# Optimization experiments

Hardware: AMD Instinct MI355X
Metric: run time of the kernel (lower is better)

The kernel has to match this reference:

```python
import jax, jax.numpy as jnp
import numpy as np

N_SRC, N_MID, N_TGT = 200000, 100000, 50000
E1, E2 = 1600000, 800000
D_IN, D_HID, D_OUT = 128, 256, 64


def setup_inputs() -> dict:
    key = jax.random.key(0)
    ks = jax.random.split(key, 10)
    x = jax.random.normal(ks[0], (N_SRC, D_IN), dtype=jnp.float32)
    # edge_index[0] = source node ids, edge_index[1] = target node ids (PyG source_to_target)
    ei1 = jnp.stack([
        jax.random.randint(ks[1], (E1,), 0, N_SRC, dtype=jnp.int32),
        jax.random.randint(ks[2], (E1,), 0, N_MID, dtype=jnp.int32),
    ])
    ei2 = jnp.stack([
        jax.random.randint(ks[3], (E2,), 0, N_MID, dtype=jnp.int32),
        jax.random.randint(ks[4], (E2,), 0, N_TGT, dtype=jnp.int32),
    ])
    s = 1.0 / np.sqrt(D_IN)
    Wl1 = jax.random.uniform(ks[5], (D_IN, D_HID), jnp.float32, -s, s)
    Wr1 = jax.random.uniform(ks[6], (D_IN, D_HID), jnp.float32, -s, s)
    b1 = jnp.zeros((D_HID,), jnp.float32)
    s2 = 1.0 / np.sqrt(D_HID)
    Wl2 = jax.random.uniform(ks[7], (D_HID, D_OUT), jnp.float32, -s2, s2)
    Wr2 = jax.random.uniform(ks[8], (D_HID, D_OUT), jnp.float32, -s2, s2)
    b2 = jnp.zeros((D_OUT,), jnp.float32)
    return {"x": x, "edge_index1": ei1, "edge_index2": ei2,
            "Wl1": Wl1, "Wr1": Wr1, "b1": b1,
            "Wl2": Wl2, "Wr2": Wr2, "b2": b2}


def _sage_conv(x_src, x_tgt, edge_index, Wl, Wr, b, n_tgt):
    # mean aggregation of source features onto targets, then two linear branches
    msg = x_src[edge_index[0]]                                   # [E, d]
    agg = jax.ops.segment_sum(msg, edge_index[1], num_segments=n_tgt)
    cnt = jax.ops.segment_sum(jnp.ones((edge_index.shape[1],), x_src.dtype),
                              edge_index[1], num_segments=n_tgt)
    agg = agg / jnp.maximum(cnt, 1.0)[:, None]
    return agg @ Wl + x_tgt @ Wr + b


def reference(x, edge_index1, edge_index2, Wl1, Wr1, b1, Wl2, Wr2, b2):
    # layer 1: [N_SRC, D_IN] -> [N_MID, D_HID], then ReLU (dropout inactive in eval)
    h = _sage_conv(x, x[:N_MID], edge_index1, Wl1, Wr1, b1, N_MID)
    h = jax.nn.relu(h)
    # layer 2 (final): no activation
    out = _sage_conv(h, h[:N_TGT], edge_index2, Wl2, Wr2, b2, N_TGT)
    return out
```

## Files before the change

### kernel.cpp

```cpp
#include <hip/hip_runtime.h>


#define NSRC 200000
#define NMID 100000
#define NTGT 50000
#define NE1  1600000
#define NE2  800000
#define DIN  128
#define DHID 256
#define DOUT 64

#define XCH (NSRC * 16)

#define CH   4096
#define NBK1 391
#define NBK2 196
#define NCH1 ((NE1 + CH - 1) / CH)
#define NCH2 ((NE2 + CH - 1) / CH)
#define HCH  8192
#define NHC1 ((NE1 + HCH - 1) / HCH)
#define NHC2 ((NE2 + HCH - 1) / HCH)
#define MAXBUF 6144

typedef __attribute__((ext_vector_type(8))) short bf16x8;
typedef __attribute__((ext_vector_type(4))) float f32x4;
typedef __attribute__((ext_vector_type(2))) float f32x2;

__device__ __forceinline__ unsigned short f2bf(float f) {
    unsigned int u = __builtin_bit_cast(unsigned int, f);
    u += 0x7FFFu + ((u >> 16) & 1u);
    return (unsigned short)(u >> 16);
}
__device__ __forceinline__ float bf_lo(unsigned int u) {
    return __builtin_bit_cast(float, u << 16);
}
__device__ __forceinline__ float bf_hi(unsigned int u) {
    return __builtin_bit_cast(float, u & 0xFFFF0000u);
}

__global__ __launch_bounds__(256) void convert_all_kernel(
    const float* __restrict__ x,
    const float* __restrict__ Wl1, const float* __restrict__ Wr1,
    const float* __restrict__ Wl2, const float* __restrict__ Wr2,
    unsigned short* __restrict__ xb, unsigned short* __restrict__ WT1,
    unsigned short* __restrict__ WT2)
{
    int gid = blockIdx.x * 256 + threadIdx.x;
    if (gid < XCH) {
        const float4 v0 = *(const float4*)(x + (long long)gid * 8);
        const float4 v1 = *(const float4*)(x + (long long)gid * 8 + 4);
        unsigned short o[8] = {f2bf(v0.x), f2bf(v0.y), f2bf(v0.z), f2bf(v0.w),
                               f2bf(v1.x), f2bf(v1.y), f2bf(v1.z), f2bf(v1.w)};
        *(uint4*)(xb + (long long)gid * 8) = *(const uint4*)o;
        return;
    }
    int g = gid - XCH;
    if (g < 65536) {
        int n = g >> 8, k = g & 255;
        float v = (k < DIN) ? Wl1[(long long)k * DHID + n]
                            : Wr1[(long long)(k - DIN) * DHID + n];
        WT1[g] = f2bf(v);
        return;
    }
    g -= 65536;
    if (g < 32768) {
        int n2 = g >> 8, k = g & 255;
        float v = (n2 < DOUT) ? Wl2[(long long)k * DOUT + n2]
                              : Wr2[(long long)k * DOUT + (n2 - DOUT)];
        WT2[g] = f2bf(v);
    }
}


__global__ __launch_bounds__(256) void bucket_hist_kernel(
    const int* __restrict__ ei1, const int* __restrict__ ei2,
    int* __restrict__ bhist1, int* __restrict__ bhist2)
{
    __shared__ unsigned int lh[512];
    const int* ei; int* bh; int nE, nbk, chunk;
    if (blockIdx.x < NHC1) { ei = ei1; bh = bhist1; nE = NE1; nbk = NBK1; chunk = blockIdx.x; }
    else { ei = ei2; bh = bhist2; nE = NE2; nbk = NBK2; chunk = blockIdx.x - NHC1; }
    int t = threadIdx.x;
    lh[t] = 0; lh[t + 256] = 0;
    __syncthreads();
    int base = chunk * HCH;
    int end = nE < base + HCH ? nE : base + HCH;
    for (int e = base + t; e < end; e += 256)
        atomicAdd(&lh[((unsigned)ei[nE + e]) >> 8], 1u);
    __syncthreads();
    if (t < nbk && lh[t]) atomicAdd(&bh[t], (int)lh[t]);
    if (t + 256 < nbk && lh[t + 256]) atomicAdd(&bh[t + 256], (int)lh[t + 256]);
}

__global__ __launch_bounds__(256) void bucket_scan_kernel(
    const int* __restrict__ bhist1, const int* __restrict__ bhist2,
    int* __restrict__ bbase1, int* __restrict__ bbase2,
    int* __restrict__ bcur1, int* __restrict__ bcur2,
    int* __restrict__ rs1, int* __restrict__ rs2)
{
    __shared__ int s[256];
    int t = threadIdx.x;
    int a0 = (2 * t < NBK1) ? bhist1[2 * t] : 0;
    int a1 = (2 * t + 1 < NBK1) ? bhist1[2 * t + 1] : 0;
    s[t] = a0 + a1;
    __syncthreads();
    for (int off = 1; off < 256; off <<= 1) {
        int u = (t >= off) ? s[t - off] : 0;
        __syncthreads();
        s[t] += u;
        __syncthreads();
    }
    int ex = (t > 0) ? s[t - 1] : 0;
    if (2 * t < NBK1)     { bbase1[2 * t] = ex;      bcur1[2 * t] = ex; }
    if (2 * t + 1 < NBK1) { bbase1[2 * t + 1] = ex + a0; bcur1[2 * t + 1] = ex + a0; }
    if (t == 0) { bbase1[NBK1] = NE1; rs1[NMID] = NE1; bbase2[NBK2] = NE2; rs2[NTGT] = NE2; }
    __syncthreads();
    int b0 = (t < NBK2) ? bhist2[t] : 0;
    s[t] = b0;
    __syncthreads();
    for (int off = 1; off < 256; off <<= 1) {
        int u = (t >= off) ? s[t - off] : 0;
        __syncthreads();
        s[t] += u;
        __syncthreads();
    }
    int ex2 = (t > 0) ? s[t - 1] : 0;
    if (t < NBK2) { bbase2[t] = ex2; bcur2[t] = ex2; }
}

__global__ __launch_bounds__(256) void bin_kernel(
    const int* __restrict__ ei1, const int* __restrict__ ei2,
    int* __restrict__ bcur1, int* __restrict__ bcur2,
    uint2* __restrict__ gbuf1, uint2* __restrict__ gbuf2)
{
    __shared__ unsigned int lcnt[512];
    __shared__ unsigned int lofs[512];
    __shared__ unsigned int lpos[512];
    __shared__ unsigned int gbase[512];
    __shared__ unsigned int swarp[256];
    __shared__ uint2 lbuf[CH];

    const int* ei; int* bcur; uint2* gbuf; int nE, nbk, chunk;
    if (blockIdx.x < NCH1) {
        ei = ei1; bcur = bcur1; gbuf = gbuf1; nE = NE1; nbk = NBK1; chunk = blockIdx.x;
    } else {
        ei = ei2; bcur = bcur2; gbuf = gbuf2; nE = NE2; nbk = NBK2; chunk = blockIdx.x - NCH1;
    }
    int base = chunk * CH;
    int nb = nE - base; if (nb > CH) nb = CH;
    int t = threadIdx.x;

    for (int i = t; i < 512; i += 256) { lcnt[i] = 0; lpos[i] = 0; }
    __syncthreads();

    int srcv[16], tgtv[16];
    #pragma unroll
    for (int i = 0; i < 16; ++i) {
        int e = base + i * 256 + t;
        if (e < nE) {
            tgtv[i] = ei[nE + e];
            srcv[i] = ei[e];
            atomicAdd(&lcnt[tgtv[i] >> 8], 1u);
        } else tgtv[i] = -1;
    }
    __syncthreads();

    unsigned a0 = lcnt[2 * t], a1 = lcnt[2 * t + 1];
    swarp[t] = a0 + a1;
    __syncthreads();
    for (int off = 1; off < 256; off <<= 1) {
        unsigned v = (t >= off) ? swarp[t - off] : 0;
        __syncthreads();
        swarp[t] += v;
        __syncthreads();
    }
    unsigned ex = (t > 0) ? swarp[t - 1] : 0;
    lofs[2 * t] = ex;
    lofs[2 * t + 1] = ex + a0;
    if (2 * t < nbk && a0) gbase[2 * t] = atomicAdd(&bcur[2 * t], (int)a0);
    if (2 * t + 1 < nbk && a1) gbase[2 * t + 1] = atomicAdd(&bcur[2 * t + 1], (int)a1);
    __syncthreads();

    #pragma unroll
    for (int i = 0; i < 16; ++i) {
        if (tgtv[i] >= 0) {
            int b = tgtv[i] >> 8;
            unsigned idx = lofs[b] + atomicAdd(&lpos[b], 1u);
            lbuf[idx] = make_uint2((unsigned)srcv[i], (unsigned)tgtv[i]);
        }
    }
    __syncthreads();

    for (int i = t; i < nb; i += 256) {
        uint2 r = lbuf[i];
        int b = (int)(r.y >> 8);
        unsigned gi = gbase[b] + ((unsigned)i - lofs[b]);
        gbuf[gi] = r;
    }
}

__global__ __launch_bounds__(256) void bucket_csr_kernel(
    const uint2* __restrict__ gbuf1, const uint2* __restrict__ gbuf2,
    const int* __restrict__ bbase1, const int* __restrict__ bbase2,
    int* __restrict__ rs1, int* __restrict__ rs2,
    int* __restrict__ csr1, int* __restrict__ csr2)
{
    __shared__ unsigned int lhist[256];
    __shared__ unsigned int lcur[256];
    __shared__ unsigned int sscan[256];
    __shared__ unsigned int lbuf[MAXBUF];
    const uint2* gbuf; const int* bbase; int* rs; int* csr; int bucket, ntot;
    if (blockIdx.x < NBK1) {
        gbuf = gbuf1; bbase = bbase1; rs = rs1; csr = csr1; bucket = blockIdx.x; ntot = NMID;
    } else {
        gbuf = gbuf2; bbase = bbase2; rs = rs2; csr = csr2; bucket = blockIdx.x - NBK1; ntot = NTGT;
    }
    int base = bbase[bucket];
    int size = bbase[bucket + 1] - base;
    int node0 = bucket << 8;
    int nnode = ntot - node0; if (nnode > 256) nnode = 256;
    int t = threadIdx.x;
    lhist[t] = 0;
    __syncthreads();
    for (int i = t; i < size; i += 256)
        atomicAdd(&lhist[gbuf[base + i].y & 255], 1u);
    __syncthreads();
    unsigned v = lhist[t];
    sscan[t] = v;
    __syncthreads();
    for (int off = 1; off < 256; off <<= 1) {
        unsigned u = (t >= off) ? sscan[t - off] : 0;
        __syncthreads();
        sscan[t] += u;
        __syncthreads();
    }
    unsigned ex = (t > 0) ? sscan[t - 1] : 0;
    lcur[t] = ex;
    if (t < nnode) rs[node0 + t] = base + (int)ex;
    __syncthreads();
    for (int i = t; i < size; i += 256) {
        uint2 r = gbuf[base + i];
        unsigned pos = atomicAdd(&lcur[r.y & 255], 1u);
        lbuf[pos] = r.x;
    }
    __syncthreads();
    for (int i = t; i < size; i += 256)
        csr[base + i] = (int)lbuf[i];
}


__global__ __launch_bounds__(256) void gather1_kernel(
    const unsigned short* __restrict__ xb, const int* __restrict__ rs,
    const int* __restrict__ csr, unsigned short* __restrict__ aggnb)
{
    int wid = threadIdx.x >> 6;
    int lane = threadIdx.x & 63;
    int node = __builtin_amdgcn_readfirstlane(blockIdx.x * 4 + wid);
    if (node >= NMID) return;
    int s = rs[node];
    int d = rs[node + 1] - s;
    const unsigned int* xw = (const unsigned int*)xb;
    f32x2 a0 = {0.f, 0.f}, a1 = {0.f, 0.f}, a2 = {0.f, 0.f}, a3 = {0.f, 0.f};
    int j = 0;
    for (; j + 3 < d; j += 4) {
        int i0 = csr[s + j];
        int i1 = csr[s + j + 1];
        int i2 = csr[s + j + 2];
        int i3 = csr[s + j + 3];
        unsigned int u0 = xw[((size_t)(unsigned)i0 << 6) + lane];
        unsigned int u1 = xw[((size_t)(unsigned)i1 << 6) + lane];
        unsigned int u2 = xw[((size_t)(unsigned)i2 << 6) + lane];
        unsigned int u3 = xw[((size_t)(unsigned)i3 << 6) + lane];
        a0 += (f32x2){bf_lo(u0), bf_hi(u0)};
        a1 += (f32x2){bf_lo(u1), bf_hi(u1)};
        a2 += (f32x2){bf_lo(u2), bf_hi(u2)};
        a3 += (f32x2){bf_lo(u3), bf_hi(u3)};
    }
    for (; j < d; ++j) {
        int i0 = csr[s + j];
        unsigned int u0 = xw[((size_t)(unsigned)i0 << 6) + lane];
        a0 += (f32x2){bf_lo(u0), bf_hi(u0)};
    }
    float inv = (d > 0) ? 1.0f / (float)d : 0.f;
    f32x2 r = (a0 + a1) + (a2 + a3);
    float r0 = r.x * inv;
    float r1 = r.y * inv;
    unsigned int packed = (unsigned int)f2bf(r0) | ((unsigned int)f2bf(r1) << 16);
    *(unsigned int*)(aggnb + (long long)node * DIN + lane * 2) = packed;
}

__global__ __launch_bounds__(256) void gather2_final_kernel(
    const float* __restrict__ p, const float* __restrict__ qb,
    const int* __restrict__ rs, const int* __restrict__ csr,
    float* __restrict__ out)
{
    int wid = threadIdx.x >> 6;
    int lane = threadIdx.x & 63;
    int node = __builtin_amdgcn_readfirstlane(blockIdx.x * 4 + wid);
    if (node >= NTGT) return;
    int s = rs[node];
    int d = rs[node + 1] - s;
    float a0 = 0.f, a1 = 0.f, a2 = 0.f, a3 = 0.f;
    int j = 0;
    for (; j + 3 < d; j += 4) {
        int i0 = csr[s + j];
        int i1 = csr[s + j + 1];
        int i2 = csr[s + j + 2];
        int i3 = csr[s + j + 3];
        a0 += p[((size_t)(unsigned)i0 << 6) + lane];
        a1 += p[((size_t)(unsigned)i1 << 6) + lane];
        a2 += p[((size_t)(unsigned)i2 << 6) + lane];
        a3 += p[((size_t)(unsigned)i3 << 6) + lane];
    }
    for (; j < d; ++j) {
        int i0 = csr[s + j];
        a0 += p[((size_t)(unsigned)i0 << 6) + lane];
    }
    float inv = (d > 0) ? 1.0f / (float)d : 0.f;
    out[(long long)node * DOUT + lane] =
        qb[(long long)node * DOUT + lane] + ((a0 + a1) + (a2 + a3)) * inv;
}

#define LDSP 40

__global__ __launch_bounds__(256) void gemm1_mfma(
    const unsigned short* __restrict__ aggnb, const unsigned short* __restrict__ xb,
    const unsigned short* __restrict__ WT, const float* __restrict__ bias,
    unsigned short* __restrict__ h)
{
    __shared__ unsigned short Asm[128 * LDSP];
    __shared__ unsigned short Bsm[128 * LDSP];
    const int tid = threadIdx.x;
    const int bm = blockIdx.x * 128;
    const int bn = blockIdx.y * 128;
    const int wave = tid >> 6, lane = tid & 63;
    const int wr = wave >> 1, wc = wave & 1;
    const int lrow = lane & 15, quad = lane >> 4;

    const int c0r = tid >> 2, c0s = tid & 3;
    const int c1r = (tid + 256) >> 2, c1s = tid & 3;
    int growA0 = bm + c0r; if (growA0 >= NMID) growA0 = NMID - 1;
    int growA1 = bm + c1r; if (growA1 >= NMID) growA1 = NMID - 1;

    uint4 pa0, pa1, pb0, pb1;
    auto gload = [&](int k0) {
        int gk0 = k0 + c0s * 8;
        const unsigned short* sA0 = (gk0 < DIN)
            ? (aggnb + (long long)growA0 * DIN + gk0)
            : (xb + (long long)growA0 * DIN + (gk0 - DIN));
        pa0 = *(const uint4*)sA0;
        const unsigned short* sA1 = (gk0 < DIN)
            ? (aggnb + (long long)growA1 * DIN + gk0)
            : (xb + (long long)growA1 * DIN + (gk0 - DIN));
        pa1 = *(const uint4*)sA1;
        pb0 = *(const uint4*)(WT + (long long)(bn + c0r) * 256 + k0 + c0s * 8);
        pb1 = *(const uint4*)(WT + (long long)(bn + c1r) * 256 + k0 + c1s * 8);
    };

    f32x4 acc[4][4];
    #pragma unroll
    for (int i = 0; i < 4; ++i)
        #pragma unroll
        for (int j = 0; j < 4; ++j)
            acc[i][j] = (f32x4){0.f, 0.f, 0.f, 0.f};

    gload(0);
    for (int it = 0; it < 8; ++it) {
        if (it) __syncthreads();
        *(uint4*)(Asm + c0r * LDSP + c0s * 8) = pa0;
        *(uint4*)(Asm + c1r * LDSP + c1s * 8) = pa1;
        *(uint4*)(Bsm + c0r * LDSP + c0s * 8) = pb0;
        *(uint4*)(Bsm + c1r * LDSP + c1s * 8) = pb1;
        __syncthreads();
        if (it < 7) gload((it + 1) * 32);
        bf16x8 af[4], bfr[4];
        #pragma unroll
        for (int mi = 0; mi < 4; ++mi)
            af[mi] = *(const bf16x8*)(Asm + (wr * 64 + mi * 16 + lrow) * LDSP + quad * 8);
        #pragma unroll
        for (int ni = 0; ni < 4; ++ni)
            bfr[ni] = *(const bf16x8*)(Bsm + (wc * 64 + ni * 16 + lrow) * LDSP + quad * 8);
        #pragma unroll
        for (int mi = 0; mi < 4; ++mi)
            #pragma unroll
            for (int ni = 0; ni < 4; ++ni)
                acc[mi][ni] = __builtin_amdgcn_mfma_f32_16x16x32_bf16(
                    af[mi], bfr[ni], acc[mi][ni], 0, 0, 0);
    }
    #pragma unroll
    for (int mi = 0; mi < 4; ++mi) {
        #pragma unroll
        for (int ni = 0; ni < 4; ++ni) {
            int col = bn + wc * 64 + ni * 16 + lrow;
            float bv = bias[col];
            #pragma unroll
            for (int r = 0; r < 4; ++r) {
                int row = bm + wr * 64 + mi * 16 + quad * 4 + r;
                if (row < NMID) {
                    float v = acc[mi][ni][r] + bv;
                    h[(long long)row * DHID + col] = f2bf(fmaxf(v, 0.0f));
                }
            }
        }
    }
}

__global__ __launch_bounds__(256) void gemm2_dual_mfma(
    const unsigned short* __restrict__ h, const unsigned short* __restrict__ WT2,
    const float* __restrict__ b2,
    float* __restrict__ p, float* __restrict__ qb)
{
    __shared__ unsigned short Asm[128 * LDSP];
    __shared__ unsigned short Bsm[128 * LDSP];
    const int tid = threadIdx.x;
    const int bm = blockIdx.x * 128;
    const int wave = tid >> 6, lane = tid & 63;
    const int lrow = lane & 15, quad = lane >> 4;
    const bool doq = (bm < NTGT);

    const int c0r = tid >> 2, c0s = tid & 3;
    const int c1r = (tid + 256) >> 2;
    int growA0 = bm + c0r; if (growA0 >= NMID) growA0 = NMID - 1;
    int growA1 = bm + c1r; if (growA1 >= NMID) growA1 = NMID - 1;

    uint4 pa0, pa1, pb0, pb1;
    auto gload = [&](int k0) {
        pa0 = *(const uint4*)(h + (long long)growA0 * DHID + k0 + c0s * 8);
        pa1 = *(const uint4*)(h + (long long)growA1 * DHID + k0 + c0s * 8);
        pb0 = *(const uint4*)(WT2 + (long long)c0r * 256 + k0 + c0s * 8);
        pb1 = *(const uint4*)(WT2 + (long long)c1r * 256 + k0 + c0s * 8);
    };

    f32x4 accP[2][4], accQ[2][4];
    #pragma unroll
    for (int i = 0; i < 2; ++i)
        #pragma unroll
        for (int j = 0; j < 4; ++j) {
            accP[i][j] = (f32x4){0.f, 0.f, 0.f, 0.f};
            accQ[i][j] = (f32x4){0.f, 0.f, 0.f, 0.f};
        }

    gload(0);
    for (int it = 0; it < 8; ++it) {
        if (it) __syncthreads();
        *(uint4*)(Asm + c0r * LDSP + c0s * 8) = pa0;
        *(uint4*)(Asm + c1r * LDSP + c0s * 8) = pa1;
        *(uint4*)(Bsm + c0r * LDSP + c0s * 8) = pb0;
        *(uint4*)(Bsm + c1r * LDSP + c0s * 8) = pb1;
        __syncthreads();
        if (it < 7) gload((it + 1) * 32);
        bf16x8 af[2], bp[4];
        #pragma unroll
        for (int mi = 0; mi < 2; ++mi)
            af[mi] = *(const bf16x8*)(Asm + (wave * 32 + mi * 16 + lrow) * LDSP + quad * 8);
        #pragma unroll
        for (int ni = 0; ni < 4; ++ni)
            bp[ni] = *(const bf16x8*)(Bsm + (ni * 16 + lrow) * LDSP + quad * 8);
        #pragma unroll
        for (int mi = 0; mi < 2; ++mi)
            #pragma unroll
            for (int ni = 0; ni < 4; ++ni)
                accP[mi][ni] = __builtin_amdgcn_mfma_f32_16x16x32_bf16(
                    af[mi], bp[ni], accP[mi][ni], 0, 0, 0);
        if (doq) {
            bf16x8 bq[4];
            #pragma unroll
            for (int ni = 0; ni < 4; ++ni)
                bq[ni] = *(const bf16x8*)(Bsm + (64 + ni * 16 + lrow) * LDSP + quad * 8);
            #pragma unroll
            for (int mi = 0; mi < 2; ++mi)
                #pragma unroll
                for (int ni = 0; ni < 4; ++ni)
                    accQ[mi][ni] = __builtin_amdgcn_mfma_f32_16x16x32_bf16(
                        af[mi], bq[ni], accQ[mi][ni], 0, 0, 0);
        }
    }
    #pragma unroll
    for (int mi = 0; mi < 2; ++mi) {
        #pragma unroll
        for (int ni = 0; ni < 4; ++ni) {
            int col = ni * 16 + lrow;
            #pragma unroll
            for (int r = 0; r < 4; ++r) {
                int row = bm + wave * 32 + mi * 16 + quad * 4 + r;
                if (row < NMID)
                    p[(long long)row * DOUT + col] = accP[mi][ni][r];
                if (doq && row < NTGT)
                    qb[(long long)row * DOUT + col] = accQ[mi][ni][r] + b2[col];
            }
        }
    }
}

extern "C" void kernel_launch(void* const* d_in, const int* in_sizes, int n_in,
                              void* d_out, int out_size, void* d_ws, size_t ws_size,
                              hipStream_t stream) {
    const float* x   = (const float*)d_in[0];
    const int*   ei1 = (const int*)d_in[1];
    const int*   ei2 = (const int*)d_in[2];
    const float* Wl1 = (const float*)d_in[3];
    const float* Wr1 = (const float*)d_in[4];
    const float* b1  = (const float*)d_in[5];
    const float* Wl2 = (const float*)d_in[6];
    const float* Wr2 = (const float*)d_in[7];
    const float* b2  = (const float*)d_in[8];
    float* out = (float*)d_out;

    unsigned short* xb    = (unsigned short*)d_ws;
    unsigned short* aggnb = xb + (size_t)NSRC * DIN;
    unsigned short* h     = aggnb + (size_t)NMID * DIN;
    unsigned short* WT1   = h + (size_t)NMID * DHID;
    unsigned short* WT2   = WT1 + 256 * 256;
    float* p    = (float*)(WT2 + 128 * 256);
    float* qb   = p + (size_t)NMID * DOUT;
    int* rs1    = (int*)(qb + (size_t)NTGT * DOUT);
    int* rs2    = rs1 + (NMID + 1);
    int* bhist1 = rs2 + (NTGT + 1);
    int* bhist2 = bhist1 + NBK1;
    int* bbase1 = bhist2 + NBK2;
    int* bbase2 = bbase1 + (NBK1 + 1);
    int* bcur1  = bbase2 + (NBK2 + 1);
    int* bcur2  = bcur1 + NBK1;
    int* csr1   = bcur2 + NBK2 + 1;
    int* csr2   = csr1 + NE1;
    uint2* gbuf1 = (uint2*)(((size_t)(csr2 + NE2) + 15) & ~(size_t)15);
    uint2* gbuf2 = gbuf1 + NE1;

    convert_all_kernel<<<(XCH + 65536 + 32768 + 255) / 256, 256, 0, stream>>>(
        x, Wl1, Wr1, Wl2, Wr2, xb, WT1, WT2);

    hipMemsetAsync(bhist1, 0, (size_t)(NBK1 + NBK2) * 4, stream);
    bucket_hist_kernel<<<NHC1 + NHC2, 256, 0, stream>>>(ei1, ei2, bhist1, bhist2);
    bucket_scan_kernel<<<1, 256, 0, stream>>>(bhist1, bhist2, bbase1, bbase2,
                                              bcur1, bcur2, rs1, rs2);
    bin_kernel<<<NCH1 + NCH2, 256, 0, stream>>>(ei1, ei2, bcur1, bcur2, gbuf1, gbuf2);
    bucket_csr_kernel<<<NBK1 + NBK2, 256, 0, stream>>>(
        gbuf1, gbuf2, bbase1, bbase2, rs1, rs2, csr1, csr2);

    gather1_kernel<<<(NMID + 3) / 4, 256, 0, stream>>>(xb, rs1, csr1, aggnb);
    {
        dim3 grid((NMID + 127) / 128, 2);
        gemm1_mfma<<<grid, 256, 0, stream>>>(aggnb, xb, WT1, b1, h);
    }
    gemm2_dual_mfma<<<(NMID + 127) / 128, 256, 0, stream>>>(h, WT2, b2, p, qb);
    gather2_final_kernel<<<(NTGT + 3) / 4, 256, 0, stream>>>(p, qb, rs2, csr2, out);
}
```

Baseline: 404.9 us.

## Make gather kernels persistent with 8-way unrolled loads and prefetched row ranges

Both gather kernels now launch a fixed grid of 2048 blocks, and each wave grid-strides over nodes instead of handling one node per wave. The next node's row start and end are prefetched while the current node is processed. The inner loop is unrolled to 8 independent loads, and the remainder is handled by a masked 8-wide tail block. This aims to raise memory-level parallelism and cut block scheduling overhead. The costs are possible over-reads of csr past a node's range, extra redundant loads in the tail, and lower occupancy.

```diff
diff --git a/kernel.cpp b/kernel.cpp
--- a/kernel.cpp
+++ b/kernel.cpp
@@ -22,6 +22,9 @@
 #define NHC2 ((NE2 + HCH - 1) / HCH)
 #define MAXBUF 6144
 
+#define GBLK 2048
+#define WSTRIDE (GBLK * 4)
+
 typedef __attribute__((ext_vector_type(8))) short bf16x8;
 typedef __attribute__((ext_vector_type(4))) float f32x4;
 typedef __attribute__((ext_vector_type(2))) float f32x2;
@@ -253,40 +256,91 @@
     const unsigned short* __restrict__ xb, const int* __restrict__ rs,
     const int* __restrict__ csr, unsigned short* __restrict__ aggnb)
 {
-    int wid = threadIdx.x >> 6;
-    int lane = threadIdx.x & 63;
-    int node = __builtin_amdgcn_readfirstlane(blockIdx.x * 4 + wid);
-    if (node >= NMID) return;
+    const int lane = threadIdx.x & 63;
+    const unsigned int* xw = (const unsigned int*)xb;
+    int nv = blockIdx.x * 4 + (threadIdx.x >> 6);
+    if (nv >= NMID) return;
+    int node = __builtin_amdgcn_readfirstlane(nv);
     int s = rs[node];
-    int d = rs[node + 1] - s;
-    const unsigned int* xw = (const unsigned int*)xb;
-    f32x2 a0 = {0.f, 0.f}, a1 = {0.f, 0.f}, a2 = {0.f, 0.f}, a3 = {0.f, 0.f};
-    int j = 0;
-    for (; j + 3 < d; j += 4) {
-        int i0 = csr[s + j];
-        int i1 = csr[s + j + 1];
-        int i2 = csr[s + j + 2];
-        int i3 = csr[s + j + 3];
-        unsigned int u0 = xw[((size_t)(unsigned)i0 << 6) + lane];
-        unsigned int u1 = xw[((size_t)(unsigned)i1 << 6) + lane];
-        unsigned int u2 = xw[((size_t)(unsigned)i2 << 6) + lane];
-        unsigned int u3 = xw[((size_t)(unsigned)i3 << 6) + lane];
-        a0 += (f32x2){bf_lo(u0), bf_hi(u0)};
-        a1 += (f32x2){bf_lo(u1), bf_hi(u1)};
-        a2 += (f32x2){bf_lo(u2), bf_hi(u2)};
-        a3 += (f32x2){bf_lo(u3), bf_hi(u3)};
-    }
-    for (; j < d; ++j) {
-        int i0 = csr[s + j];
-        unsigned int u0 = xw[((size_t)(unsigned)i0 << 6) + lane];
-        a0 += (f32x2){bf_lo(u0), bf_hi(u0)};
-    }
-    float inv = (d > 0) ? 1.0f / (float)d : 0.f;
-    f32x2 r = (a0 + a1) + (a2 + a3);
-    float r0 = r.x * inv;
-    float r1 = r.y * inv;
-    unsigned int packed = (unsigned int)f2bf(r0) | ((unsigned int)f2bf(r1) << 16);
-    *(unsigned int*)(aggnb + (long long)node * DIN + lane * 2) = packed;
+    int e = rs[node + 1];
+    while (true) {
+        int nvn = nv + WSTRIDE;
+        int sn = 0, en = 0;
+        if (nvn < NMID) {
+            int nn = __builtin_amdgcn_readfirstlane(nvn);
+            sn = rs[nn];
+            en = rs[nn + 1];
+        }
+        int d = e - s;
+        f32x2 a0 = {0.f,0.f}, a1 = {0.f,0.f}, a2 = {0.f,0.f}, a3 = {0.f,0.f};
+        f32x2 a4 = {0.f,0.f}, a5 = {0.f,0.f}, a6 = {0.f,0.f}, a7 = {0.f,0.f};
+        int j = 0;
+        for (; j + 8 <= d; j += 8) {
+            int i0 = csr[s + j + 0], i1 = csr[s + j + 1];
+            int i2 = csr[s + j + 2], i3 = csr[s + j + 3];
+            int i4 = csr[s + j + 4], i5 = csr[s + j + 5];
+            int i6 = csr[s + j + 6], i7 = csr[s + j + 7];
+            unsigned u0 = xw[((size_t)(unsigned)i0 << 6) + lane];
+            unsigned u1 = xw[((size_t)(unsigned)i1 << 6) + lane];
+            unsigned u2 = xw[((size_t)(unsigned)i2 << 6) + lane];
+            unsigned u3 = xw[((size_t)(unsigned)i3 << 6) + lane];
+            unsigned u4 = xw[((size_t)(unsigned)i4 << 6) + lane];
+            unsigned u5 = xw[((size_t)(unsigned)i5 << 6) + lane];
+            unsigned u6 = xw[((size_t)(unsigned)i6 << 6) + lane];
+            unsigned u7 = xw[((size_t)(unsigned)i7 << 6) + lane];
+            a0 += (f32x2){bf_lo(u0), bf_hi(u0)};
+            a1 += (f32x2){bf_lo(u1), bf_hi(u1)};
+            a2 += (f32x2){bf_lo(u2), bf_hi(u2)};
+            a3 += (f32x2){bf_lo(u3), bf_hi(u3)};
+            a4 += (f32x2){bf_lo(u4), bf_hi(u4)};
+            a5 += (f32x2){bf_lo(u5), bf_hi(u5)};
+            a6 += (f32x2){bf_lo(u6), bf_hi(u6)};
+            a7 += (f32x2){bf_lo(u7), bf_hi(u7)};
+        }
+        if (j < d) {
+            int nb = d - j;
+            int i0 = csr[s + j + 0];
+            int i1r = csr[s + j + 1], i2r = csr[s + j + 2], i3r = csr[s + j + 3];
+            int i4r = csr[s + j + 4], i5r = csr[s + j + 5], i6r = csr[s + j + 6];
+            int i7r = csr[s + j + 7];
+            int i1 = (1 < nb) ? i1r : i0;
+            int i2 = (2 < nb) ? i2r : i0;
+            int i3 = (3 < nb) ? i3r : i0;
+            int i4 = (4 < nb) ? i4r : i0;
+            int i5 = (5 < nb) ? i5r : i0;
+            int i6 = (6 < nb) ? i6r : i0;
+            int i7 = (7 < nb) ? i7r : i0;
+            unsigned u0 = xw[((size_t)(unsigned)i0 << 6) + lane];
+            unsigned u1 = xw[((size_t)(unsigned)i1 << 6) + lane];
+            unsigned u2 = xw[((size_t)(unsigned)i2 << 6) + lane];
+            unsigned u3 = xw[((size_t)(unsigned)i3 << 6) + lane];
+            unsigned u4 = xw[((size_t)(unsigned)i4 << 6) + lane];
+            unsigned u5 = xw[((size_t)(unsigned)i5 << 6) + lane];
+            unsigned u6 = xw[((size_t)(unsigned)i6 << 6) + lane];
+            unsigned u7 = xw[((size_t)(unsigned)i7 << 6) + lane];
+            float w1 = (1 < nb) ? 1.f : 0.f, w2 = (2 < nb) ? 1.f : 0.f;
+            float w3 = (3 < nb) ? 1.f : 0.f, w4 = (4 < nb) ? 1.f : 0.f;
+            float w5 = (5 < nb) ? 1.f : 0.f, w6 = (6 < nb) ? 1.f : 0.f;
+            float w7 = (7 < nb) ? 1.f : 0.f;
+            a0 += (f32x2){bf_lo(u0), bf_hi(u0)};
+            a1 += (f32x2){bf_lo(u1), bf_hi(u1)} * w1;
+            a2 += (f32x2){bf_lo(u2), bf_hi(u2)} * w2;
+            a3 += (f32x2){bf_lo(u3), bf_hi(u3)} * w3;
+            a4 += (f32x2){bf_lo(u4), bf_hi(u4)} * w4;
+            a5 += (f32x2){bf_lo(u5), bf_hi(u5)} * w5;
+            a6 += (f32x2){bf_lo(u6), bf_hi(u6)} * w6;
+            a7 += (f32x2){bf_lo(u7), bf_hi(u7)} * w7;
+        }
+        float inv = (d > 0) ? 1.0f / (float)d : 0.f;
+        f32x2 r = ((a0 + a1) + (a2 + a3)) + ((a4 + a5) + (a6 + a7));
+        unsigned int packed =
+            (unsigned int)f2bf(r.x * inv) | ((unsigned int)f2bf(r.y * inv) << 16);
+        *(unsigned int*)(aggnb + (long long)node * DIN + lane * 2) = packed;
+        if (nvn >= NMID) break;
+        nv = nvn;
+        node = __builtin_amdgcn_readfirstlane(nvn);
+        s = sn; e = en;
+    }
 }
 
 __global__ __launch_bounds__(256) void gather2_final_kernel(
@@ -294,31 +348,73 @@
     const int* __restrict__ rs, const int* __restrict__ csr,
     float* __restrict__ out)
 {
-    int wid = threadIdx.x >> 6;
-    int lane = threadIdx.x & 63;
-    int node = __builtin_amdgcn_readfirstlane(blockIdx.x * 4 + wid);
-    if (node >= NTGT) return;
+    const int lane = threadIdx.x & 63;
+    int nv = blockIdx.x * 4 + (threadIdx.x >> 6);
+    if (nv >= NTGT) return;
+    int node = __builtin_amdgcn_readfirstlane(nv);
     int s = rs[node];
-    int d = rs[node + 1] - s;
-    float a0 = 0.f, a1 = 0.f, a2 = 0.f, a3 = 0.f;
-    int j = 0;
-    for (; j + 3 < d; j += 4) {
-        int i0 = csr[s + j];
-        int i1 = csr[s + j + 1];
-        int i2 = csr[s + j + 2];
-        int i3 = csr[s + j + 3];
-        a0 += p[((size_t)(unsigned)i0 << 6) + lane];
-        a1 += p[((size_t)(unsigned)i1 << 6) + lane];
-        a2 += p[((size_t)(unsigned)i2 << 6) + lane];
-        a3 += p[((size_t)(unsigned)i3 << 6) + lane];
-    }
-    for (; j < d; ++j) {
-        int i0 = csr[s + j];
-        a0 += p[((size_t)(unsigned)i0 << 6) + lane];
-    }
-    float inv = (d > 0) ? 1.0f / (float)d : 0.f;
-    out[(long long)node * DOUT + lane] =
-        qb[(long long)node * DOUT + lane] + ((a0 + a1) + (a2 + a3)) * inv;
+    int e = rs[node + 1];
+    while (true) {
+        int nvn = nv + WSTRIDE;
+        int sn = 0, en = 0;
+        if (nvn < NTGT) {
+            int nn = __builtin_amdgcn_readfirstlane(nvn);
+            sn = rs[nn];
+            en = rs[nn + 1];
+        }
+        int d = e - s;
+        float a0 = 0.f, a1 = 0.f, a2 = 0.f, a3 = 0.f;
+        float a4 = 0.f, a5 = 0.f, a6 = 0.f, a7 = 0.f;
+        int j = 0;
+        for (; j + 8 <= d; j += 8) {
+            int i0 = csr[s + j + 0], i1 = csr[s + j + 1];
+            int i2 = csr[s + j + 2], i3 = csr[s + j + 3];
+            int i4 = csr[s + j + 4], i5 = csr[s + j + 5];
+            int i6 = csr[s + j + 6], i7 = csr[s + j + 7];
+            a0 += p[((size_t)(unsigned)i0 << 6) + lane];
+            a1 += p[((size_t)(unsigned)i1 << 6) + lane];
+            a2 += p[((size_t)(unsigned)i2 << 6) + lane];
+            a3 += p[((size_t)(unsigned)i3 << 6) + lane];
+            a4 += p[((size_t)(unsigned)i4 << 6) + lane];
+            a5 += p[((size_t)(unsigned)i5 << 6) + lane];
+            a6 += p[((size_t)(unsigned)i6 << 6) + lane];
+            a7 += p[((size_t)(unsigned)i7 << 6) + lane];
+        }
+        if (j < d) {
+            int nb = d - j;
+            int i0 = csr[s + j + 0];
+            int i1r = csr[s + j + 1], i2r = csr[s + j + 2], i3r = csr[s + j + 3];
+            int i4r = csr[s + j + 4], i5r = csr[s + j + 5], i6r = csr[s + j + 6];
+            int i7r = csr[s + j + 7];
+            int i1 = (1 < nb) ? i1r : i0;
+            int i2 = (2 < nb) ? i2r : i0;
+            int i3 = (3 < nb) ? i3r : i0;
+            int i4 = (4 < nb) ? i4r : i0;
+            int i5 = (5 < nb) ? i5r : i0;
+            int i6 = (6 < nb) ? i6r : i0;
+            int i7 = (7 < nb) ? i7r : i0;
+            float w1 = (1 < nb) ? 1.f : 0.f, w2 = (2 < nb) ? 1.f : 0.f;
+            float w3 = (3 < nb) ? 1.f : 0.f, w4 = (4 < nb) ? 1.f : 0.f;
+            float w5 = (5 < nb) ? 1.f : 0.f, w6 = (6 < nb) ? 1.f : 0.f;
+            float w7 = (7 < nb) ? 1.f : 0.f;
+            a0 += p[((size_t)(unsigned)i0 << 6) + lane];
+            a1 += p[((size_t)(unsigned)i1 << 6) + lane] * w1;
+            a2 += p[((size_t)(unsigned)i2 << 6) + lane] * w2;
+            a3 += p[((size_t)(unsigned)i3 << 6) + lane] * w3;
+            a4 += p[((size_t)(unsigned)i4 << 6) + lane] * w4;
+            a5 += p[((size_t)(unsigned)i5 << 6) + lane] * w5;
+            a6 += p[((size_t)(unsigned)i6 << 6) + lane] * w6;
+            a7 += p[((size_t)(unsigned)i7 << 6) + lane] * w7;
+        }
+        float inv = (d > 0) ? 1.0f / (float)d : 0.f;
+        out[(long long)node * DOUT + lane] =
+            qb[(long long)node * DOUT + lane] +
+            (((a0 + a1) + (a2 + a3)) + ((a4 + a5) + (a6 + a7))) * inv;
+        if (nvn >= NTGT) break;
+        nv = nvn;
+        node = __builtin_amdgcn_readfirstlane(nvn);
+        s = sn; e = en;
+    }
 }
 
 #define LDSP 40
@@ -537,11 +633,11 @@
     bucket_csr_kernel<<<NBK1 + NBK2, 256, 0, stream>>>(
         gbuf1, gbuf2, bbase1, bbase2, rs1, rs2, csr1, csr2);
 
-    gather1_kernel<<<(NMID + 3) / 4, 256, 0, stream>>>(xb, rs1, csr1, aggnb);
+    gather1_kernel<<<GBLK, 256, 0, stream>>>(xb, rs1, csr1, aggnb);
     {
         dim3 grid((NMID + 127) / 128, 2);
         gemm1_mfma<<<grid, 256, 0, stream>>>(aggnb, xb, WT1, b1, h);
     }
     gemm2_dual_mfma<<<(NMID + 127) / 128, 256, 0, stream>>>(h, WT2, b2, p, qb);
-    gather2_final_kernel<<<(NTGT + 3) / 4, 256, 0, stream>>>(p, qb, rs2, csr2, out);
-}
+    gather2_final_kernel<<<GBLK, 256, 0, stream>>>(p, qb, rs2, csr2, out);
+}
```

Result: no change. 405.9 us (+0.2%).
